# Performance work log

Hardware: AMD Instinct MI355X
Metric: run time of the kernel (lower is better)

The kernel has to match this reference:

```python
import jax, jax.numpy as jnp
import numpy as np

B, D, C, E, H = 65536, 512, 101, 8, 256


def setup_inputs() -> dict:
    key = jax.random.key(0)
    ks = jax.random.split(key, 7)
    s_d = 1.0 / np.sqrt(D)
    s_h = 1.0 / np.sqrt(H)
    return {
        "x": jax.random.normal(ks[0], (B, D), dtype=jnp.float32),
        "W1": jax.random.uniform(ks[1], (E, D, H), jnp.float32, -s_d, s_d),  # expert layer1
        "b1": jax.random.uniform(ks[2], (E, H), jnp.float32, -s_d, s_d),
        "W2": jax.random.uniform(ks[3], (E, H, C), jnp.float32, -s_h, s_h),  # expert layer2
        "b2": jax.random.uniform(ks[4], (E, C), jnp.float32, -s_h, s_h),
        "Wg": jax.random.uniform(ks[5], (D, E), jnp.float32, -s_d, s_d),     # gate
        "bg": jax.random.uniform(ks[6], (E,), jnp.float32, -s_d, s_d),
    }


def reference(x, W1, b1, W2, b2, Wg, bg):
    # gate: softmax over experts
    gates = jax.nn.softmax(x @ Wg + bg, axis=1)                 # [B, E]
    # all experts: batched two-layer MLP
    h = jax.nn.relu(jnp.einsum("bd,edh->beh", x, W1) + b1)      # [B, E, H]
    eo = jnp.einsum("beh,ehc->bec", h, W2) + b2                 # [B, E, C]
    # gate-weighted sum over experts
    return jnp.einsum("be,bec->bc", gates, eo)                  # [B, C]
```

## Files before the change

### kernel.cpp

```cpp
#include <hip/hip_runtime.h>


typedef __attribute__((ext_vector_type(8))) short short8x;
typedef __attribute__((ext_vector_type(4))) float float4x;

#define C_DIM 101

__device__ __forceinline__ unsigned short f2bf(float f) {
  unsigned int u = __builtin_bit_cast(unsigned int, f);
  u += 0x7fffu + ((u >> 16) & 1u);
  return (unsigned short)(u >> 16);
}

__global__ void conv_w1(const float* __restrict__ W1, const float* __restrict__ Wg,
                        unsigned short* __restrict__ out) {
  int s = blockIdx.x * blockDim.x + threadIdx.x;
  int l = s & 63;
  int frag = s >> 6;
  int kf = frag & 15;
  int ntile = frag >> 4;
  int n = (ntile << 4) | (l & 15);
  int k = (kf << 5) | ((l >> 4) << 3);
  short8x v;
#pragma unroll
  for (int j = 0; j < 8; ++j) {
    int kk = k + j;
    float f;
    if (n < 2048)      f = W1[((size_t)(n >> 8) * 512 + kk) * 256 + (n & 255)];
    else if (n < 2056) f = Wg[(size_t)kk * 8 + (n - 2048)];
    else               f = 0.f;
    v[j] = (short)f2bf(f);
  }
  *(short8x*)(out + (size_t)s * 8) = v;
}

__global__ void conv_w2(const float* __restrict__ W2, unsigned short* __restrict__ out) {
  int s = blockIdx.x * blockDim.x + threadIdx.x;
  int l = s & 63;
  int frag = s >> 6;
  int kf = frag & 63;
  int ntile = frag >> 6;
  int c = (ntile << 4) | (l & 15);
  int k = (kf << 5) | ((l >> 4) << 3);
  short8x v;
#pragma unroll
  for (int j = 0; j < 8; ++j) {
    int kk = k + j;
    float f = (c < C_DIM) ? W2[((size_t)(kk >> 8) * 256 + (kk & 255)) * C_DIM + c] : 0.f;
    v[j] = (short)f2bf(f);
  }
  *(short8x*)(out + (size_t)s * 8) = v;
}

__global__ __launch_bounds__(512, 4) void moe_main(
    const float* __restrict__ x, const float* __restrict__ b1,
    const float* __restrict__ b2, const float* __restrict__ bg,
    const unsigned short* __restrict__ W1bf, const unsigned short* __restrict__ W2bf,
    float* __restrict__ out) {
  __shared__ unsigned short xA[32 * 512];
  __shared__ unsigned short hA[32 * 512];
  __shared__ float gt[8 * 32];
  float* graw = (float*)hA;

  const int tid = threadIdx.x;
  const int w = tid >> 6;
  const int l = tid & 63;
  const int quad = l >> 4;
  const int p = l & 15;
  const int r0 = blockIdx.x * 32;

#pragma unroll
  for (int it = 0; it < 4; ++it) {
    int g = tid + it * 512;
    int m = g >> 6;
    int k0 = (g & 63) << 3;
    const float* src = x + (size_t)(r0 + m) * 512 + k0;
    float4 f0 = *(const float4*)src;
    float4 f1 = *(const float4*)(src + 4);
    short8x v;
    v[0] = (short)f2bf(f0.x); v[1] = (short)f2bf(f0.y);
    v[2] = (short)f2bf(f0.z); v[3] = (short)f2bf(f0.w);
    v[4] = (short)f2bf(f1.x); v[5] = (short)f2bf(f1.y);
    v[6] = (short)f2bf(f1.z); v[7] = (short)f2bf(f1.w);
    int mt = m >> 4;
    int kfrag = k0 >> 5;
    int lane = (((k0 >> 3) & 3) << 4) | (m & 15);
    *(short8x*)&xA[(size_t)(((mt << 4) | kfrag) * 64 + lane) * 8] = v;
  }
  __syncthreads();

  if (w < 2) {
    float4x acc = {0.f, 0.f, 0.f, 0.f};
#pragma unroll 2
    for (int kf = 0; kf < 16; ++kf) {
      short8x a = *(const short8x*)&xA[(size_t)((w * 16 + kf) * 64 + l) * 8];
      short8x b = *(const short8x*)(W1bf + ((size_t)(128 * 16 + kf) * 512 + l * 8));
      acc = __builtin_amdgcn_mfma_f32_16x16x32_bf16(a, b, acc, 0, 0, 0);
    }
    if (p < 8) {
      float bgv = bg[p];
#pragma unroll
      for (int r = 0; r < 4; ++r)
        graw[(w * 16 + quad * 4 + r) * 8 + p] = acc[r] + bgv;
    }
  }
  __syncthreads();
  if (tid < 32) {
    float v[8], mx = -1e30f;
#pragma unroll
    for (int e = 0; e < 8; ++e) { v[e] = graw[tid * 8 + e]; mx = fmaxf(mx, v[e]); }
    float s = 0.f;
#pragma unroll
    for (int e = 0; e < 8; ++e) { v[e] = expf(v[e] - mx); s += v[e]; }
    float inv = 1.f / s;
#pragma unroll
    for (int e = 0; e < 8; ++e) gt[e * 32 + tid] = v[e] * inv;
  }
  __syncthreads();

  float4x zero = {0.f, 0.f, 0.f, 0.f};
  float4x acc2[2];
  acc2[0] = zero; acc2[1] = zero;

  for (int it = 0; it < 4; ++it) {
#pragma unroll
    for (int eo = 0; eo < 2; ++eo) {
      const int e = it * 2 + eo;
      float4x acc1[2][2];
      acc1[0][0] = zero; acc1[0][1] = zero; acc1[1][0] = zero; acc1[1][1] = zero;

      const unsigned short* __restrict__ bp =
          W1bf + ((size_t)(e * 16 + w * 2) * 16) * 512 + (size_t)l * 8;
      short8x bA0 = *(const short8x*)(bp);
      short8x bA1 = *(const short8x*)(bp + 8192);
      short8x bB0, bB1;
#pragma unroll
      for (int kf = 0; kf < 16; kf += 2) {
        bB0 = *(const short8x*)(bp + (kf + 1) * 512);
        bB1 = *(const short8x*)(bp + 8192 + (kf + 1) * 512);
        short8x a0 = *(const short8x*)&xA[(size_t)((0 * 16 + kf) * 64 + l) * 8];
        short8x a1 = *(const short8x*)&xA[(size_t)((1 * 16 + kf) * 64 + l) * 8];
        acc1[0][0] = __builtin_amdgcn_mfma_f32_16x16x32_bf16(a0, bA0, acc1[0][0], 0, 0, 0);
        acc1[1][0] = __builtin_amdgcn_mfma_f32_16x16x32_bf16(a1, bA0, acc1[1][0], 0, 0, 0);
        acc1[0][1] = __builtin_amdgcn_mfma_f32_16x16x32_bf16(a0, bA1, acc1[0][1], 0, 0, 0);
        acc1[1][1] = __builtin_amdgcn_mfma_f32_16x16x32_bf16(a1, bA1, acc1[1][1], 0, 0, 0);
        if (kf + 2 < 16) {
          bA0 = *(const short8x*)(bp + (kf + 2) * 512);
          bA1 = *(const short8x*)(bp + 8192 + (kf + 2) * 512);
        }
        short8x a2 = *(const short8x*)&xA[(size_t)((0 * 16 + kf + 1) * 64 + l) * 8];
        short8x a3 = *(const short8x*)&xA[(size_t)((1 * 16 + kf + 1) * 64 + l) * 8];
        acc1[0][0] = __builtin_amdgcn_mfma_f32_16x16x32_bf16(a2, bB0, acc1[0][0], 0, 0, 0);
        acc1[1][0] = __builtin_amdgcn_mfma_f32_16x16x32_bf16(a3, bB0, acc1[1][0], 0, 0, 0);
        acc1[0][1] = __builtin_amdgcn_mfma_f32_16x16x32_bf16(a2, bB1, acc1[0][1], 0, 0, 0);
        acc1[1][1] = __builtin_amdgcn_mfma_f32_16x16x32_bf16(a3, bB1, acc1[1][1], 0, 0, 0);
      }

      if (eo == 0) __syncthreads();

      float4x gv0 = *(const float4x*)&gt[e * 32 + 0  + quad * 4];
      float4x gv1 = *(const float4x*)&gt[e * 32 + 16 + quad * 4];
#pragma unroll
      for (int nc = 0; nc < 2; ++nc) {
        int cw = w * 32 + nc * 16 + p;
        float b1v = b1[e * 256 + cw];
        int jj = p & 7;
        int ldbase = ((nc * 2 + (p >> 3)) << 4);
#pragma unroll
        for (int mt = 0; mt < 2; ++mt) {
#pragma unroll
          for (int r = 0; r < 4; ++r) {
            float hv = fmaxf(acc1[mt][nc][r] + b1v, 0.f) * (mt ? gv1[r] : gv0[r]);
            hA[(size_t)((eo * 16 + w * 2 + mt) * 512) + (ldbase + quad * 4 + r) * 8 + jj] =
                f2bf(hv);
          }
        }
      }
    }
    __syncthreads();

    if (w < 7) {
      const unsigned short* __restrict__ bp2 =
          W2bf + ((size_t)(w * 64 + it * 16)) * 512 + (size_t)l * 8;
#pragma unroll
      for (int eo = 0; eo < 2; ++eo) {
#pragma unroll
        for (int kk = 0; kk < 8; ++kk) {
          short8x a0 = *(const short8x*)&hA[(size_t)((eo * 16 + kk * 2 + 0) * 64 + l) * 8];
          short8x a1 = *(const short8x*)&hA[(size_t)((eo * 16 + kk * 2 + 1) * 64 + l) * 8];
          short8x b = *(const short8x*)(bp2 + (size_t)(eo * 8 + kk) * 512);
          acc2[0] = __builtin_amdgcn_mfma_f32_16x16x32_bf16(a0, b, acc2[0], 0, 0, 0);
          acc2[1] = __builtin_amdgcn_mfma_f32_16x16x32_bf16(a1, b, acc2[1], 0, 0, 0);
        }
      }
    }
  }

  if (w < 7) {
    int c = w * 16 + p;
    if (c < C_DIM) {
#pragma unroll
      for (int mt = 0; mt < 2; ++mt) {
#pragma unroll
        for (int r = 0; r < 4; ++r) {
          int row = mt * 16 + quad * 4 + r;
          float bias = 0.f;
#pragma unroll
          for (int e = 0; e < 8; ++e) bias += gt[e * 32 + row] * b2[e * C_DIM + c];
          out[(size_t)(r0 + row) * C_DIM + c] = acc2[mt][r] + bias;
        }
      }
    }
  }
}

extern "C" void kernel_launch(void* const* d_in, const int* in_sizes, int n_in,
                              void* d_out, int out_size, void* d_ws, size_t ws_size,
                              hipStream_t stream) {
  const float* x  = (const float*)d_in[0];
  const float* W1 = (const float*)d_in[1];
  const float* b1 = (const float*)d_in[2];
  const float* W2 = (const float*)d_in[3];
  const float* b2 = (const float*)d_in[4];
  const float* Wg = (const float*)d_in[5];
  const float* bg = (const float*)d_in[6];
  float* out = (float*)d_out;

  unsigned short* W1bf = (unsigned short*)d_ws;
  unsigned short* W2bf = (unsigned short*)((char*)d_ws + (size_t)129 * 16 * 512 * 2);

  conv_w1<<<516, 256, 0, stream>>>(W1, Wg, W1bf);
  conv_w2<<<128, 256, 0, stream>>>(W2, W2bf);
  moe_main<<<2048, 512, 0, stream>>>(x, b1, b2, bg, W1bf, W2bf, out);
}
```

Before: 403.3 us.

## Double rows per block to 64 and merge weight conversion kernels

Each workgroup now processes 64 rows instead of 32, so every bf16 weight fragment loaded from global memory feeds four MFMA row tiles instead of two. This halves weight traffic per output row. The two weight-conversion kernels are merged into a single launch to cut launch overhead. The cost is doubled LDS use (about 130KB), which lowers occupancy, and more accumulator registers per thread.

```diff
diff --git a/kernel.cpp b/kernel.cpp
--- a/kernel.cpp
+++ b/kernel.cpp
@@ -12,54 +12,56 @@
   return (unsigned short)(u >> 16);
 }
 
-__global__ void conv_w1(const float* __restrict__ W1, const float* __restrict__ Wg,
-                        unsigned short* __restrict__ out) {
-  int s = blockIdx.x * blockDim.x + threadIdx.x;
-  int l = s & 63;
-  int frag = s >> 6;
-  int kf = frag & 15;
-  int ntile = frag >> 4;
-  int n = (ntile << 4) | (l & 15);
-  int k = (kf << 5) | ((l >> 4) << 3);
-  short8x v;
-#pragma unroll
-  for (int j = 0; j < 8; ++j) {
-    int kk = k + j;
-    float f;
-    if (n < 2048)      f = W1[((size_t)(n >> 8) * 512 + kk) * 256 + (n & 255)];
-    else if (n < 2056) f = Wg[(size_t)kk * 8 + (n - 2048)];
-    else               f = 0.f;
-    v[j] = (short)f2bf(f);
-  }
-  *(short8x*)(out + (size_t)s * 8) = v;
-}
-
-__global__ void conv_w2(const float* __restrict__ W2, unsigned short* __restrict__ out) {
-  int s = blockIdx.x * blockDim.x + threadIdx.x;
-  int l = s & 63;
-  int frag = s >> 6;
-  int kf = frag & 63;
-  int ntile = frag >> 6;
-  int c = (ntile << 4) | (l & 15);
-  int k = (kf << 5) | ((l >> 4) << 3);
-  short8x v;
-#pragma unroll
-  for (int j = 0; j < 8; ++j) {
-    int kk = k + j;
-    float f = (c < C_DIM) ? W2[((size_t)(kk >> 8) * 256 + (kk & 255)) * C_DIM + c] : 0.f;
-    v[j] = (short)f2bf(f);
-  }
-  *(short8x*)(out + (size_t)s * 8) = v;
-}
-
-__global__ __launch_bounds__(512, 4) void moe_main(
+__global__ void conv_weights(const float* __restrict__ W1, const float* __restrict__ Wg,
+                             const float* __restrict__ W2,
+                             unsigned short* __restrict__ W1bf,
+                             unsigned short* __restrict__ W2bf) {
+  if (blockIdx.x < 516) {
+    int s = blockIdx.x * blockDim.x + threadIdx.x;
+    int l = s & 63;
+    int frag = s >> 6;
+    int kf = frag & 15;
+    int ntile = frag >> 4;
+    int n = (ntile << 4) | (l & 15);
+    int k = (kf << 5) | ((l >> 4) << 3);
+    short8x v;
+#pragma unroll
+    for (int j = 0; j < 8; ++j) {
+      int kk = k + j;
+      float f;
+      if (n < 2048)      f = W1[((size_t)(n >> 8) * 512 + kk) * 256 + (n & 255)];
+      else if (n < 2056) f = Wg[(size_t)kk * 8 + (n - 2048)];
+      else               f = 0.f;
+      v[j] = (short)f2bf(f);
+    }
+    *(short8x*)(W1bf + (size_t)s * 8) = v;
+  } else {
+    int s = (blockIdx.x - 516) * blockDim.x + threadIdx.x;
+    int l = s & 63;
+    int frag = s >> 6;
+    int kf = frag & 63;
+    int ntile = frag >> 6;
+    int c = (ntile << 4) | (l & 15);
+    int k = (kf << 5) | ((l >> 4) << 3);
+    short8x v;
+#pragma unroll
+    for (int j = 0; j < 8; ++j) {
+      int kk = k + j;
+      float f = (c < C_DIM) ? W2[((size_t)(kk >> 8) * 256 + (kk & 255)) * C_DIM + c] : 0.f;
+      v[j] = (short)f2bf(f);
+    }
+    *(short8x*)(W2bf + (size_t)s * 8) = v;
+  }
+}
+
+__global__ __launch_bounds__(512, 2) void moe_main(
     const float* __restrict__ x, const float* __restrict__ b1,
     const float* __restrict__ b2, const float* __restrict__ bg,
     const unsigned short* __restrict__ W1bf, const unsigned short* __restrict__ W2bf,
     float* __restrict__ out) {
-  __shared__ unsigned short xA[32 * 512];
-  __shared__ unsigned short hA[32 * 512];
-  __shared__ float gt[8 * 32];
+  __shared__ unsigned short xA[64 * 512];
+  __shared__ unsigned short hA[64 * 512];
+  __shared__ float gt[8 * 64];
   float* graw = (float*)hA;
 
   const int tid = threadIdx.x;
@@ -67,10 +69,10 @@
   const int l = tid & 63;
   const int quad = l >> 4;
   const int p = l & 15;
-  const int r0 = blockIdx.x * 32;
-
-#pragma unroll
-  for (int it = 0; it < 4; ++it) {
+  const int r0 = blockIdx.x * 64;
+
+#pragma unroll
+  for (int it = 0; it < 8; ++it) {
     int g = tid + it * 512;
     int m = g >> 6;
     int k0 = (g & 63) << 3;
@@ -89,7 +91,7 @@
   }
   __syncthreads();
 
-  if (w < 2) {
+  if (w < 4) {
     float4x acc = {0.f, 0.f, 0.f, 0.f};
 #pragma unroll 2
     for (int kf = 0; kf < 16; ++kf) {
@@ -105,7 +107,7 @@
     }
   }
   __syncthreads();
-  if (tid < 32) {
+  if (tid < 64) {
     float v[8], mx = -1e30f;
 #pragma unroll
     for (int e = 0; e < 8; ++e) { v[e] = graw[tid * 8 + e]; mx = fmaxf(mx, v[e]); }
@@ -114,20 +116,21 @@
     for (int e = 0; e < 8; ++e) { v[e] = expf(v[e] - mx); s += v[e]; }
     float inv = 1.f / s;
 #pragma unroll
-    for (int e = 0; e < 8; ++e) gt[e * 32 + tid] = v[e] * inv;
+    for (int e = 0; e < 8; ++e) gt[e * 64 + tid] = v[e] * inv;
   }
   __syncthreads();
 
   float4x zero = {0.f, 0.f, 0.f, 0.f};
-  float4x acc2[2];
-  acc2[0] = zero; acc2[1] = zero;
+  float4x acc2[4];
+  acc2[0] = zero; acc2[1] = zero; acc2[2] = zero; acc2[3] = zero;
 
   for (int it = 0; it < 4; ++it) {
 #pragma unroll
     for (int eo = 0; eo < 2; ++eo) {
       const int e = it * 2 + eo;
-      float4x acc1[2][2];
-      acc1[0][0] = zero; acc1[0][1] = zero; acc1[1][0] = zero; acc1[1][1] = zero;
+      float4x acc1[4][2];
+#pragma unroll
+      for (int mt = 0; mt < 4; ++mt) { acc1[mt][0] = zero; acc1[mt][1] = zero; }
 
       const unsigned short* __restrict__ bp =
           W1bf + ((size_t)(e * 16 + w * 2) * 16) * 512 + (size_t)l * 8;
@@ -138,28 +141,30 @@
       for (int kf = 0; kf < 16; kf += 2) {
         bB0 = *(const short8x*)(bp + (kf + 1) * 512);
         bB1 = *(const short8x*)(bp + 8192 + (kf + 1) * 512);
-        short8x a0 = *(const short8x*)&xA[(size_t)((0 * 16 + kf) * 64 + l) * 8];
-        short8x a1 = *(const short8x*)&xA[(size_t)((1 * 16 + kf) * 64 + l) * 8];
-        acc1[0][0] = __builtin_amdgcn_mfma_f32_16x16x32_bf16(a0, bA0, acc1[0][0], 0, 0, 0);
-        acc1[1][0] = __builtin_amdgcn_mfma_f32_16x16x32_bf16(a1, bA0, acc1[1][0], 0, 0, 0);
-        acc1[0][1] = __builtin_amdgcn_mfma_f32_16x16x32_bf16(a0, bA1, acc1[0][1], 0, 0, 0);
-        acc1[1][1] = __builtin_amdgcn_mfma_f32_16x16x32_bf16(a1, bA1, acc1[1][1], 0, 0, 0);
+#pragma unroll
+        for (int mt = 0; mt < 4; ++mt) {
+          short8x a = *(const short8x*)&xA[(size_t)((mt * 16 + kf) * 64 + l) * 8];
+          acc1[mt][0] = __builtin_amdgcn_mfma_f32_16x16x32_bf16(a, bA0, acc1[mt][0], 0, 0, 0);
+          acc1[mt][1] = __builtin_amdgcn_mfma_f32_16x16x32_bf16(a, bA1, acc1[mt][1], 0, 0, 0);
+        }
         if (kf + 2 < 16) {
           bA0 = *(const short8x*)(bp + (kf + 2) * 512);
           bA1 = *(const short8x*)(bp + 8192 + (kf + 2) * 512);
         }
-        short8x a2 = *(const short8x*)&xA[(size_t)((0 * 16 + kf + 1) * 64 + l) * 8];
-        short8x a3 = *(const short8x*)&xA[(size_t)((1 * 16 + kf + 1) * 64 + l) * 8];
-        acc1[0][0] = __builtin_amdgcn_mfma_f32_16x16x32_bf16(a2, bB0, acc1[0][0], 0, 0, 0);
-        acc1[1][0] = __builtin_amdgcn_mfma_f32_16x16x32_bf16(a3, bB0, acc1[1][0], 0, 0, 0);
-        acc1[0][1] = __builtin_amdgcn_mfma_f32_16x16x32_bf16(a2, bB1, acc1[0][1], 0, 0, 0);
-        acc1[1][1] = __builtin_amdgcn_mfma_f32_16x16x32_bf16(a3, bB1, acc1[1][1], 0, 0, 0);
+#pragma unroll
+        for (int mt = 0; mt < 4; ++mt) {
+          short8x a = *(const short8x*)&xA[(size_t)((mt * 16 + kf + 1) * 64 + l) * 8];
+          acc1[mt][0] = __builtin_amdgcn_mfma_f32_16x16x32_bf16(a, bB0, acc1[mt][0], 0, 0, 0);
+          acc1[mt][1] = __builtin_amdgcn_mfma_f32_16x16x32_bf16(a, bB1, acc1[mt][1], 0, 0, 0);
+        }
       }
 
       if (eo == 0) __syncthreads();
 
-      float4x gv0 = *(const float4x*)&gt[e * 32 + 0  + quad * 4];
-      float4x gv1 = *(const float4x*)&gt[e * 32 + 16 + quad * 4];
+      float4x gv0 = *(const float4x*)&gt[e * 64 + 0  + quad * 4];
+      float4x gv1 = *(const float4x*)&gt[e * 64 + 16 + quad * 4];
+      float4x gv2 = *(const float4x*)&gt[e * 64 + 32 + quad * 4];
+      float4x gv3 = *(const float4x*)&gt[e * 64 + 48 + quad * 4];
 #pragma unroll
       for (int nc = 0; nc < 2; ++nc) {
         int cw = w * 32 + nc * 16 + p;
@@ -167,11 +172,12 @@
         int jj = p & 7;
         int ldbase = ((nc * 2 + (p >> 3)) << 4);
 #pragma unroll
-        for (int mt = 0; mt < 2; ++mt) {
+        for (int mt = 0; mt < 4; ++mt) {
+          float4x gv = (mt == 0) ? gv0 : (mt == 1) ? gv1 : (mt == 2) ? gv2 : gv3;
 #pragma unroll
           for (int r = 0; r < 4; ++r) {
-            float hv = fmaxf(acc1[mt][nc][r] + b1v, 0.f) * (mt ? gv1[r] : gv0[r]);
-            hA[(size_t)((eo * 16 + w * 2 + mt) * 512) + (ldbase + quad * 4 + r) * 8 + jj] =
+            float hv = fmaxf(acc1[mt][nc][r] + b1v, 0.f) * gv[r];
+            hA[(size_t)((eo * 32 + w * 4 + mt) * 512) + (ldbase + quad * 4 + r) * 8 + jj] =
                 f2bf(hv);
           }
         }
@@ -185,12 +191,13 @@
 #pragma unroll
       for (int eo = 0; eo < 2; ++eo) {
 #pragma unroll
-        for (int kk = 0; kk < 8; ++kk) {
-          short8x a0 = *(const short8x*)&hA[(size_t)((eo * 16 + kk * 2 + 0) * 64 + l) * 8];
-          short8x a1 = *(const short8x*)&hA[(size_t)((eo * 16 + kk * 2 + 1) * 64 + l) * 8];
-          short8x b = *(const short8x*)(bp2 + (size_t)(eo * 8 + kk) * 512);
-          acc2[0] = __builtin_amdgcn_mfma_f32_16x16x32_bf16(a0, b, acc2[0], 0, 0, 0);
-          acc2[1] = __builtin_amdgcn_mfma_f32_16x16x32_bf16(a1, b, acc2[1], 0, 0, 0);
+        for (int kf2 = 0; kf2 < 8; ++kf2) {
+          short8x b = *(const short8x*)(bp2 + (size_t)(eo * 8 + kf2) * 512);
+#pragma unroll
+          for (int mt = 0; mt < 4; ++mt) {
+            short8x a = *(const short8x*)&hA[(size_t)((eo * 32 + kf2 * 4 + mt) * 64 + l) * 8];
+            acc2[mt] = __builtin_amdgcn_mfma_f32_16x16x32_bf16(a, b, acc2[mt], 0, 0, 0);
+          }
         }
       }
     }
@@ -200,13 +207,13 @@
     int c = w * 16 + p;
     if (c < C_DIM) {
 #pragma unroll
-      for (int mt = 0; mt < 2; ++mt) {
+      for (int mt = 0; mt < 4; ++mt) {
 #pragma unroll
         for (int r = 0; r < 4; ++r) {
           int row = mt * 16 + quad * 4 + r;
           float bias = 0.f;
 #pragma unroll
-          for (int e = 0; e < 8; ++e) bias += gt[e * 32 + row] * b2[e * C_DIM + c];
+          for (int e = 0; e < 8; ++e) bias += gt[e * 64 + row] * b2[e * C_DIM + c];
           out[(size_t)(r0 + row) * C_DIM + c] = acc2[mt][r] + bias;
         }
       }
@@ -229,7 +236,6 @@
   unsigned short* W1bf = (unsigned short*)d_ws;
   unsigned short* W2bf = (unsigned short*)((char*)d_ws + (size_t)129 * 16 * 512 * 2);
 
-  conv_w1<<<516, 256, 0, stream>>>(W1, Wg, W1bf);
-  conv_w2<<<128, 256, 0, stream>>>(W2, W2bf);
-  moe_main<<<2048, 512, 0, stream>>>(x, b1, b2, bg, W1bf, W2bf, out);
-}
+  conv_weights<<<644, 256, 0, stream>>>(W1, Wg, W2, W1bf, W2bf);
+  moe_main<<<1024, 512, 0, stream>>>(x, b1, b2, bg, W1bf, W2bf, out);
+}
```

Measured after the change: 399.3 us. Within noise of the previous version (-1.0%).
